# Kernel tuning notes

Hardware: AMD Instinct MI355X
Metric: run time of the kernel (lower is better)

The kernel has to match this reference:

```python
import jax, jax.numpy as jnp
import numpy as np

# Loihi neuron / simulation constants (params['neuron'], params['simulation'])
VTH_MANT = 80
V_DECAY = 128
I_DECAY = 1024
REF_DELAY = 1
WGT_EXP = 0
TAU_RHO = 1.0
SCALE_RHO = 1.0
TS = 1
THETA = float(VTH_MANT * (1 << 6))      # 5120, Loihi threshold in fixed-point units
W_SCALE = float(1 << (6 + WGT_EXP))     # 64, weight scaling into Loihi fixed point


def st_floor(x):
    """floor with straight-through gradient (Loihi integer truncation)."""
    return x + jax.lax.stop_gradient(jnp.floor(x) - x)


@jax.custom_vjp
def spike_fn(v):
    # binary spike scaled by 1/Ts, as in SLAYER-Loihi
    return (v >= THETA).astype(v.dtype) * (1.0 / TS)

def _spike_fwd(v):
    return spike_fn(v), v

def _spike_bwd(v, g):
    # SLAYER surrogate: scaleRho/(tauRho*theta) * exp(-|v - theta| / (tauRho*theta))
    pdf = (SCALE_RHO / (TAU_RHO * THETA)) * jnp.exp(-jnp.abs(v - THETA) / (TAU_RHO * THETA))
    return (g * pdf,)

spike_fn.defvjp(_spike_fwd, _spike_bwd)


def quantize_w(w, step=2.0):
    """SLAYER snn.utils.quantize(w, 2) with straight-through gradient."""
    return w + jax.lax.stop_gradient(jnp.round(w / step) * step - w)


def loihi_spikes(wsp):
    """Loihi CUBA neuron scan. wsp: [T, B, C] weighted spike input -> [T, B, C] spikes."""
    i_mul = (4096.0 - I_DECAY) / 4096.0
    v_mul = (4096.0 - V_DECAY) / 4096.0

    def step(carry, x):
        I, V, ref = carry
        I = st_floor(I * i_mul) + W_SCALE * x
        V = st_floor(V * v_mul) + I
        V = jnp.where(ref > 0, jnp.zeros_like(V), V)   # refractory hold at 0
        s = spike_fn(V)
        V = V * (1.0 - s * TS)                          # reset to 0 on spike
        ref = jnp.where(s > 0, REF_DELAY - 1, jnp.maximum(ref - 1, 0))
        return (I, V, ref), s

    B, C = wsp.shape[1], wsp.shape[2]
    init = (jnp.zeros((B, C), wsp.dtype),
            jnp.zeros((B, C), wsp.dtype),
            jnp.zeros((B, C), jnp.int32))
    _, s = jax.lax.scan(step, init, wsp)
    return s


def delay_shift(x):
    """delayShift(x, 1): shift spikes one step forward in time. x: [T, B, C]."""
    return jnp.concatenate([jnp.zeros_like(x[:1]), x[:-1]], axis=0)


def setup_inputs() -> dict:
    key = jax.random.key(0)
    k1, k2, k3 = jax.random.split(key, 3)
    B, IN, HID, OUT, T = 32, 1024, 2048, 512, 256
    spike_input = (jax.random.uniform(k1, (B, IN, T)) < 0.05).astype(jnp.float32)
    W1 = jax.random.normal(k2, (HID, IN), jnp.float32) * 8.0
    W2 = jax.random.normal(k3, (OUT, HID), jnp.float32) * 8.0
    return {"spike_input": spike_input, "W1": W1, "W2": W2}


def reference(spike_input, W1, W2):
    # spike_input: [B, IN, T] binary spikes
    x = jnp.transpose(spike_input, (2, 0, 1))          # [T, B, IN]
    w1 = quantize_w(W1)
    w2 = quantize_w(W2)
    h = jnp.einsum('tbi,hi->tbh', x, w1)               # fc1 per timestep
    s1 = delay_shift(loihi_spikes(h))                  # spikeLoihi + delayShift(1)
    o = jnp.einsum('tbh,oh->tbo', s1, w2)              # fc2 per timestep
    s2 = delay_shift(loihi_spikes(o))
    return jnp.transpose(s2, (1, 2, 0))                # [B, OUT, T]
```

## Files before the change

### kernel.cpp

```cpp
#include <hip/hip_runtime.h>

typedef unsigned char u8;
typedef signed char i8;
typedef unsigned int u32;
typedef __attribute__((ext_vector_type(4))) int i32x4;

#define AS1 __attribute__((address_space(1)))
#define AS3 __attribute__((address_space(3)))

__device__ __forceinline__ void gload_lds16(const void* g, void* l) {
    __builtin_amdgcn_global_load_lds((const AS1 void*)g, (AS3 void*)l, 16, 0, 0);
}

__global__ void prep(const float* __restrict__ X, i8* __restrict__ Xb,
                     const float4* __restrict__ W1, const float4* __restrict__ W2,
                     char4* __restrict__ W1q, char4* __restrict__ W2q) {
    const int n1v = 2048 * 1024 / 4, n2v = 512 * 2048 / 4;
    __shared__ float tile[128][33];
    int bid = blockIdx.x;
    if (bid < 3072) {
        int i = bid * 256 + threadIdx.x;
        if (i < n1v) {
            float4 w = W1[i];
            char4 q;
            q.x = (i8)(int)rintf(w.x * 0.5f);
            q.y = (i8)(int)rintf(w.y * 0.5f);
            q.z = (i8)(int)rintf(w.z * 0.5f);
            q.w = (i8)(int)rintf(w.w * 0.5f);
            W1q[i] = q;
        } else {
            int j = i - n1v;
            if (j < n2v) {
                float4 w = W2[j];
                char4 q;
                q.x = (i8)(int)rintf(w.x * 0.5f);
                q.y = (i8)(int)rintf(w.y * 0.5f);
                q.z = (i8)(int)rintf(w.z * 0.5f);
                q.w = (i8)(int)rintf(w.w * 0.5f);
                W2q[j] = q;
            }
        }
        return;
    }
    bid -= 3072;
    const int B = 32, IN = 1024, T = 256;
    const int t0 = (bid & 7) * 32, i0 = ((bid >> 3) & 7) * 128, b = bid >> 6;
    const int tx = threadIdx.x & 31, ty = threadIdx.x >> 5;
    const float* src = X + (size_t)b * IN * T;
#pragma unroll
    for (int r = 0; r < 16; ++r) {
        int i = ty + r * 8;
        tile[i][tx] = src[(size_t)(i0 + i) * T + t0 + tx];
    }
    __syncthreads();
    const int cx = threadIdx.x & 31;
    const int tl0 = threadIdx.x >> 5;
#pragma unroll
    for (int r = 0; r < 4; ++r) {
        int tl = tl0 + r * 8;
        uchar4 pk;
        pk.x = (tile[cx * 4 + 0][tl] != 0.f) ? 1 : 0;
        pk.y = (tile[cx * 4 + 1][tl] != 0.f) ? 1 : 0;
        pk.z = (tile[cx * 4 + 2][tl] != 0.f) ? 1 : 0;
        pk.w = (tile[cx * 4 + 3][tl] != 0.f) ? 1 : 0;
        *(uchar4*)&Xb[((size_t)b * T + t0 + tl) * IN + i0 + cx * 4] = pk;
    }
}

__global__ __launch_bounds__(512, 4) void gemm1_scan1(
        const i8* __restrict__ A, const i8* __restrict__ Bt,
        i8* __restrict__ S1, int K) {
    __shared__ __align__(16) i8 lds[69632];
    i8*    lA   = lds;
    i8*    lB   = lds + 32768;
    short* hT   = (short*)lds;
    u32*   bits = (u32*)(lds + 65536);

    const int nwg = gridDim.x;
    const int cpx = nwg >> 3;
    const int wg  = (blockIdx.x & 7) * cpx + (blockIdx.x >> 3);
    const int bx = wg & 15;
    const int by = wg >> 4;
    const int n0 = bx * 128;
    const int m0 = by * 256;

    const int tid  = threadIdx.x;
    const int lane = tid & 63;
    const int w    = tid >> 6;
    const int wm   = w & 3;
    const int wn   = w >> 2;
    const int l15 = lane & 15;
    const int l4  = lane >> 4;
    const int sw  = l15 & 7;

    i32x4 acc[4][4] = {};
    const int flatT = tid * 16;

    for (int k0 = 0; k0 < K; k0 += 128) {
        __syncthreads();
#pragma unroll
        for (int q = 0; q < 4; ++q) {
            int fl = q * 8192 + flatT;
            int r  = fl >> 7;
            int sc = ((fl >> 4) & 7) ^ (r & 7);
            gload_lds16(A + (size_t)(m0 + r) * K + k0 + sc * 16, &lA[fl]);
        }
#pragma unroll
        for (int q = 0; q < 2; ++q) {
            int fl = q * 8192 + flatT;
            int r  = fl >> 7;
            int sc = ((fl >> 4) & 7) ^ (r & 7);
            gload_lds16(Bt + (size_t)(n0 + r) * K + k0 + sc * 16, &lB[fl]);
        }
        __syncthreads();
#pragma unroll
        for (int kk = 0; kk < 2; ++kk) {
            i32x4 af[4], bf[4];
#pragma unroll
            for (int mf = 0; mf < 4; ++mf)
                af[mf] = *(const i32x4*)&lA[(wm * 64 + mf * 16 + l15) * 128 +
                                            ((kk * 4 + l4) ^ sw) * 16];
#pragma unroll
            for (int nf = 0; nf < 4; ++nf)
                bf[nf] = *(const i32x4*)&lB[(wn * 64 + nf * 16 + l15) * 128 +
                                            ((kk * 4 + l4) ^ sw) * 16];
#pragma unroll
            for (int mf = 0; mf < 4; ++mf)
#pragma unroll
                for (int nf = 0; nf < 4; ++nf)
                    acc[mf][nf] = __builtin_amdgcn_mfma_i32_16x16x64_i8(
                        af[mf], bf[nf], acc[mf][nf], 0, 0, 0);
        }
    }
    __syncthreads();

#pragma unroll
    for (int mf = 0; mf < 4; ++mf)
#pragma unroll
        for (int nf = 0; nf < 4; ++nf) {
            int n = wn * 64 + nf * 16 + l15;
            int c = wm * 16 + mf * 4 + l4;
            int h0 = acc[mf][nf][0] * 2, h1 = acc[mf][nf][1] * 2;
            int h2 = acc[mf][nf][2] * 2, h3 = acc[mf][nf][3] * 2;
            int2 pk;
            pk.x = (h0 & 0xffff) | (h1 << 16);
            pk.y = (h2 & 0xffff) | (h3 << 16);
            *(int2*)((char*)hT + n * 512 + ((c ^ (n & 15)) << 3)) = pk;
        }
    __syncthreads();

    {
        const int ssel = blockIdx.x & 3;
        const int w1   = 4 + ((ssel + 1) & 3);
        const int nbase = (w == ssel) ? 0 : (w == w1) ? 64 : -1;
        if (nbase >= 0) {
            const int n = nbase + lane;
            const int nx = n & 15;
            const char* hrow = (char*)hT + n * 512;
            int2 ra[4], rb[4];
#pragma unroll
            for (int q = 0; q < 4; ++q)
                ra[q] = *(const int2*)(hrow + ((q ^ nx) << 3));
            u32 bw[8] = {0, 0, 0, 0, 0, 0, 0, 0};
            float I = 0.f, V = 0.f;
#pragma unroll
            for (int p = 0; p < 16; ++p) {
                if (p < 15) {
#pragma unroll
                    for (int q = 0; q < 4; ++q) {
                        int2 v = *(const int2*)(hrow + ((((p + 1) * 4 + q) ^ nx) << 3));
                        if (p & 1) ra[q] = v; else rb[q] = v;
                    }
                }
#pragma unroll
                for (int q = 0; q < 4; ++q) {
                    int2 hh = (p & 1) ? rb[q] : ra[q];
#pragma unroll
                    for (int j = 0; j < 4; ++j) {
                        int t = p * 16 + q * 4 + j;
                        short hv = (j == 0) ? (short)hh.x
                                 : (j == 1) ? (short)(hh.x >> 16)
                                 : (j == 2) ? (short)hh.y
                                            : (short)(hh.y >> 16);
                        I = floorf(I * 0.75f) + 64.f * (float)hv;
                        V = floorf(V * 0.96875f) + I;
                        if (V >= 5120.f) { bw[t >> 5] |= (1u << (t & 31)); V = 0.f; }
                    }
                }
            }
#pragma unroll
            for (int wi = 0; wi < 8; ++wi) bits[wi * 128 + n] = bw[wi];
        }
    }
    __syncthreads();

#pragma unroll
    for (int rep = 0; rep < 16; ++rep) {
        int d   = rep * 512 + tid;
        int tt  = d >> 5;
        int ndq = d & 31;
        u32 outw = 0;
        if (tt > 0) {
            int tb = tt - 1, wi = tb >> 5, sh = tb & 31;
            outw =  ((bits[wi * 128 + ndq * 4 + 0] >> sh) & 1)
                 | (((bits[wi * 128 + ndq * 4 + 1] >> sh) & 1) << 8)
                 | (((bits[wi * 128 + ndq * 4 + 2] >> sh) & 1) << 16)
                 | (((bits[wi * 128 + ndq * 4 + 3] >> sh) & 1) << 24);
        }
        *(u32*)&S1[(size_t)(m0 + tt) * 2048 + n0 + ndq * 4] = outw;
    }
}

__global__ __launch_bounds__(512, 2) void gemm2_scan2(
        const i8* __restrict__ A, const i8* __restrict__ Bt,
        float* __restrict__ out) {
    const int K = 2048;
    __shared__ __align__(16) i8 lds[81920];
    float* hT   = (float*)lds;
    u32*   bits = (u32*)(lds + 65536);

    const int nwg = gridDim.x;
    const int cpx = nwg >> 3;
    const int wg  = (blockIdx.x & 7) * cpx + (blockIdx.x >> 3);
    const int scanw = blockIdx.x & 7;
    const int ox = wg & 7;
    const int by = wg >> 3;
    const int n0 = ox * 64;
    const int m0 = by * 256;

    const int tid  = threadIdx.x;
    const int lane = tid & 63;
    const int w    = tid >> 6;
    const int wm   = w & 3;
    const int wn   = w >> 2;
    const int l15 = lane & 15;
    const int l4  = lane >> 4;
    const int sw  = l15 & 7;

    i32x4 acc[4][2] = {};

    auto STAGE = [&](int buf, int k0) {
        i8* lA = lds + buf * 40960;
        i8* lB = lA + 32768;
#pragma unroll
        for (int q = 0; q < 4; ++q) {
            int fl = q * 8192 + tid * 16;
            int r  = fl >> 7;
            int sc = ((fl >> 4) & 7) ^ (r & 7);
            gload_lds16(A + (size_t)(m0 + r) * K + k0 + sc * 16, &lA[fl]);
        }
        {
            int fl = tid * 16;
            int r  = fl >> 7;
            int sc = ((fl >> 4) & 7) ^ (r & 7);
            gload_lds16(Bt + (size_t)(n0 + r) * K + k0 + sc * 16, &lB[fl]);
        }
    };

    auto COMPUTE = [&](int buf) {
        const i8* lA = lds + buf * 40960;
        const i8* lB = lA + 32768;
#pragma unroll
        for (int kk = 0; kk < 2; ++kk) {
            i32x4 af[4], bf[2];
#pragma unroll
            for (int mf = 0; mf < 4; ++mf)
                af[mf] = *(const i32x4*)&lA[(wm * 64 + mf * 16 + l15) * 128 +
                                            ((kk * 4 + l4) ^ sw) * 16];
#pragma unroll
            for (int nf = 0; nf < 2; ++nf)
                bf[nf] = *(const i32x4*)&lB[(wn * 32 + nf * 16 + l15) * 128 +
                                            ((kk * 4 + l4) ^ sw) * 16];
#pragma unroll
            for (int mf = 0; mf < 4; ++mf)
#pragma unroll
                for (int nf = 0; nf < 2; ++nf)
                    acc[mf][nf] = __builtin_amdgcn_mfma_i32_16x16x64_i8(
                        af[mf], bf[nf], acc[mf][nf], 0, 0, 0);
        }
    };

    STAGE(0, 0);
    __syncthreads();
    int cur = 0;
    for (int k0 = 0; k0 < K; k0 += 128) {
        if (k0 + 128 < K) STAGE(cur ^ 1, k0 + 128);
        COMPUTE(cur);
        __syncthreads();
        cur ^= 1;
    }

#pragma unroll
    for (int mf = 0; mf < 4; ++mf)
#pragma unroll
        for (int nf = 0; nf < 2; ++nf) {
            int n = wn * 32 + nf * 16 + l15;
            int c = wm * 16 + mf * 4 + l4;
            float4 pk;
            pk.x = (float)(acc[mf][nf][0] * 2);
            pk.y = (float)(acc[mf][nf][1] * 2);
            pk.z = (float)(acc[mf][nf][2] * 2);
            pk.w = (float)(acc[mf][nf][3] * 2);
            *(float4*)((char*)hT + n * 1024 + ((c ^ (n & 15)) << 4)) = pk;
        }
    __syncthreads();

    if (w == scanw) {
        const int n = lane;
        const int nx = n & 15;
        const char* hrow = (char*)hT + n * 1024;
        float4 ra[4], rb[4];
#pragma unroll
        for (int q = 0; q < 4; ++q)
            ra[q] = *(const float4*)(hrow + ((q ^ nx) << 4));
        u32 bw[8] = {0, 0, 0, 0, 0, 0, 0, 0};
        float I = 0.f, V = 0.f;
#pragma unroll
        for (int p = 0; p < 16; ++p) {
            if (p < 15) {
#pragma unroll
                for (int q = 0; q < 4; ++q) {
                    float4 v = *(const float4*)(hrow + ((((p + 1) * 4 + q) ^ nx) << 4));
                    if (p & 1) ra[q] = v; else rb[q] = v;
                }
            }
#pragma unroll
            for (int q = 0; q < 4; ++q) {
                float4 hh = (p & 1) ? rb[q] : ra[q];
#pragma unroll
                for (int j = 0; j < 4; ++j) {
                    int t = p * 16 + q * 4 + j;
                    float hv = (j == 0) ? hh.x : (j == 1) ? hh.y
                             : (j == 2) ? hh.z : hh.w;
                    I = floorf(I * 0.75f) + 64.f * hv;
                    V = floorf(V * 0.96875f) + I;
                    if (V >= 5120.f) { bw[t >> 5] |= (1u << (t & 31)); V = 0.f; }
                }
            }
        }
#pragma unroll
        for (int wi = 0; wi < 8; ++wi) bits[wi * 64 + n] = bw[wi];
    }
    __syncthreads();

#pragma unroll
    for (int rep = 0; rep < 8; ++rep) {
        int flat = rep * 512 + tid;
        int o  = flat >> 6;
        int t4 = flat & 63;
        float4 v;
#pragma unroll
        for (int j = 0; j < 4; ++j) {
            int tt = t4 * 4 + j;
            float s = 0.f;
            if (tt > 0) {
                int tb = tt - 1;
                s = (float)((bits[(tb >> 5) * 64 + o] >> (tb & 31)) & 1);
            }
            if (j == 0) v.x = s; else if (j == 1) v.y = s;
            else if (j == 2) v.z = s; else v.w = s;
        }
        *(float4*)&out[((size_t)by * 512 + n0 + o) * 256 + t4 * 4] = v;
    }
}

extern "C" void kernel_launch(void* const* d_in, const int* in_sizes, int n_in,
                              void* d_out, int out_size, void* d_ws, size_t ws_size,
                              hipStream_t stream) {
    const int B = 32, IN = 1024, HID = 2048, OUT = 512, T = 256;
    const float* spikes = (const float*)d_in[0];
    const float* W1 = (const float*)d_in[1];
    const float* W2 = (const float*)d_in[2];
    float* out = (float*)d_out;

    char* ws = (char*)d_ws;
    size_t off = 0;
    auto alloc = [&](size_t bytes) -> void* {
        void* p = ws + off;
        off += (bytes + 255) & ~(size_t)255;
        return p;
    };
    i8* Xb  = (i8*)alloc((size_t)B * T * IN);
    i8* W1q = (i8*)alloc((size_t)HID * IN);
    i8* W2q = (i8*)alloc((size_t)OUT * HID);
    i8* S1  = (i8*)alloc((size_t)B * T * HID);

    prep<<<dim3(5120), dim3(256), 0, stream>>>(
        spikes, Xb, (const float4*)W1, (const float4*)W2,
        (char4*)W1q, (char4*)W2q);
    gemm1_scan1<<<dim3(512), dim3(512), 0, stream>>>(Xb, W1q, S1, IN);
    gemm2_scan2<<<dim3(256), dim3(512), 0, stream>>>(S1, W2q, out);
}
```

Before: 62.16 us.

## Triple-buffer GEMM1 K-loop with async LDS loads and vmcnt waits

Replaces the single-buffered 128-wide K loop in gemm1_scan1 with a three-stage ring of 64-wide K tiles. Global-to-LDS loads are issued three tiles ahead and waited on with explicit vmcnt counts, so memory latency overlaps MFMA work. The loop is fully unrolled with a hardcoded K=1024, uses a new XOR swizzle and raises wave priority around the MFMA groups. LDS use grows to 77824 bytes, which may cut occupancy, and the kernel now works only for K=1024.

```diff
diff --git a/kernel.cpp b/kernel.cpp
--- a/kernel.cpp
+++ b/kernel.cpp
@@ -10,6 +10,13 @@
 
 __device__ __forceinline__ void gload_lds16(const void* g, void* l) {
     __builtin_amdgcn_global_load_lds((const AS1 void*)g, (AS3 void*)l, 16, 0, 0);
+}
+
+template <int N>
+__device__ __forceinline__ void vm_wait() {
+    if constexpr (N == 0)      asm volatile("s_waitcnt vmcnt(0)" ::: "memory");
+    else if constexpr (N == 3) asm volatile("s_waitcnt vmcnt(3)" ::: "memory");
+    else if constexpr (N == 6) asm volatile("s_waitcnt vmcnt(6)" ::: "memory");
 }
 
 __global__ void prep(const float* __restrict__ X, i8* __restrict__ Xb,
@@ -69,12 +76,11 @@
 
 __global__ __launch_bounds__(512, 4) void gemm1_scan1(
         const i8* __restrict__ A, const i8* __restrict__ Bt,
-        i8* __restrict__ S1, int K) {
-    __shared__ __align__(16) i8 lds[69632];
-    i8*    lA   = lds;
-    i8*    lB   = lds + 32768;
+        i8* __restrict__ S1) {
+    const int K = 1024;
+    __shared__ __align__(16) i8 lds[77824];
     short* hT   = (short*)lds;
-    u32*   bits = (u32*)(lds + 65536);
+    u32*   bits = (u32*)(lds + 73728);
 
     const int nwg = gridDim.x;
     const int cpx = nwg >> 3;
@@ -91,46 +97,78 @@
     const int wn   = w >> 2;
     const int l15 = lane & 15;
     const int l4  = lane >> 4;
-    const int sw  = l15 & 7;
+    const int sw  = (l15 >> 1) & 3;
 
     i32x4 acc[4][4] = {};
-    const int flatT = tid * 16;
-
-    for (int k0 = 0; k0 < K; k0 += 128) {
-        __syncthreads();
-#pragma unroll
-        for (int q = 0; q < 4; ++q) {
-            int fl = q * 8192 + flatT;
-            int r  = fl >> 7;
-            int sc = ((fl >> 4) & 7) ^ (r & 7);
+
+    auto STAGE = [&](int p, int kt) {
+        i8* lA = lds + p * 24576;
+        i8* lB = lA + 16384;
+        const int k0 = kt * 64;
+#pragma unroll
+        for (int q = 0; q < 2; ++q) {
+            int fl = q * 8192 + tid * 16;
+            int r  = fl >> 6;
+            int sc = ((fl >> 4) & 3) ^ ((r >> 1) & 3);
             gload_lds16(A + (size_t)(m0 + r) * K + k0 + sc * 16, &lA[fl]);
         }
-#pragma unroll
-        for (int q = 0; q < 2; ++q) {
-            int fl = q * 8192 + flatT;
-            int r  = fl >> 7;
-            int sc = ((fl >> 4) & 7) ^ (r & 7);
+        {
+            int fl = tid * 16;
+            int r  = fl >> 6;
+            int sc = ((fl >> 4) & 3) ^ ((r >> 1) & 3);
             gload_lds16(Bt + (size_t)(n0 + r) * K + k0 + sc * 16, &lB[fl]);
         }
-        __syncthreads();
-#pragma unroll
-        for (int kk = 0; kk < 2; ++kk) {
-            i32x4 af[4], bf[4];
-#pragma unroll
-            for (int mf = 0; mf < 4; ++mf)
-                af[mf] = *(const i32x4*)&lA[(wm * 64 + mf * 16 + l15) * 128 +
-                                            ((kk * 4 + l4) ^ sw) * 16];
-#pragma unroll
-            for (int nf = 0; nf < 4; ++nf)
-                bf[nf] = *(const i32x4*)&lB[(wn * 64 + nf * 16 + l15) * 128 +
-                                            ((kk * 4 + l4) ^ sw) * 16];
-#pragma unroll
-            for (int mf = 0; mf < 4; ++mf)
-#pragma unroll
-                for (int nf = 0; nf < 4; ++nf)
-                    acc[mf][nf] = __builtin_amdgcn_mfma_i32_16x16x64_i8(
-                        af[mf], bf[nf], acc[mf][nf], 0, 0, 0);
-        }
+    };
+
+    STAGE(0, 0);
+    STAGE(1, 1);
+    STAGE(2, 2);
+
+#pragma unroll
+    for (int t = 0; t < 16; ++t) {
+        if (t <= 13)      vm_wait<6>();
+        else if (t == 14) vm_wait<3>();
+        else              vm_wait<0>();
+        __builtin_amdgcn_s_barrier();
+        __builtin_amdgcn_sched_barrier(0);
+
+        const i8* lA = lds + (t % 3) * 24576;
+        const i8* lB = lA + 16384;
+        const int co = ((l4 ^ sw) << 4);
+
+        i32x4 bf0 = *(const i32x4*)&lB[(wn * 64 +  0 + l15) * 64 + co];
+        i32x4 bf1 = *(const i32x4*)&lB[(wn * 64 + 16 + l15) * 64 + co];
+        i32x4 bf2 = *(const i32x4*)&lB[(wn * 64 + 32 + l15) * 64 + co];
+        i32x4 bf3 = *(const i32x4*)&lB[(wn * 64 + 48 + l15) * 64 + co];
+        i32x4 af0 = *(const i32x4*)&lA[(wm * 64 +  0 + l15) * 64 + co];
+        i32x4 af1 = *(const i32x4*)&lA[(wm * 64 + 16 + l15) * 64 + co];
+        __builtin_amdgcn_s_setprio(1);
+        acc[0][0] = __builtin_amdgcn_mfma_i32_16x16x64_i8(af0, bf0, acc[0][0], 0, 0, 0);
+        acc[0][1] = __builtin_amdgcn_mfma_i32_16x16x64_i8(af0, bf1, acc[0][1], 0, 0, 0);
+        acc[0][2] = __builtin_amdgcn_mfma_i32_16x16x64_i8(af0, bf2, acc[0][2], 0, 0, 0);
+        acc[0][3] = __builtin_amdgcn_mfma_i32_16x16x64_i8(af0, bf3, acc[0][3], 0, 0, 0);
+        acc[1][0] = __builtin_amdgcn_mfma_i32_16x16x64_i8(af1, bf0, acc[1][0], 0, 0, 0);
+        acc[1][1] = __builtin_amdgcn_mfma_i32_16x16x64_i8(af1, bf1, acc[1][1], 0, 0, 0);
+        acc[1][2] = __builtin_amdgcn_mfma_i32_16x16x64_i8(af1, bf2, acc[1][2], 0, 0, 0);
+        acc[1][3] = __builtin_amdgcn_mfma_i32_16x16x64_i8(af1, bf3, acc[1][3], 0, 0, 0);
+        __builtin_amdgcn_s_setprio(0);
+
+        i32x4 af2 = *(const i32x4*)&lA[(wm * 64 + 32 + l15) * 64 + co];
+        i32x4 af3 = *(const i32x4*)&lA[(wm * 64 + 48 + l15) * 64 + co];
+        __builtin_amdgcn_s_setprio(1);
+        acc[2][0] = __builtin_amdgcn_mfma_i32_16x16x64_i8(af2, bf0, acc[2][0], 0, 0, 0);
+        acc[2][1] = __builtin_amdgcn_mfma_i32_16x16x64_i8(af2, bf1, acc[2][1], 0, 0, 0);
+        acc[2][2] = __builtin_amdgcn_mfma_i32_16x16x64_i8(af2, bf2, acc[2][2], 0, 0, 0);
+        acc[2][3] = __builtin_amdgcn_mfma_i32_16x16x64_i8(af2, bf3, acc[2][3], 0, 0, 0);
+        acc[3][0] = __builtin_amdgcn_mfma_i32_16x16x64_i8(af3, bf0, acc[3][0], 0, 0, 0);
+        acc[3][1] = __builtin_amdgcn_mfma_i32_16x16x64_i8(af3, bf1, acc[3][1], 0, 0, 0);
+        acc[3][2] = __builtin_amdgcn_mfma_i32_16x16x64_i8(af3, bf2, acc[3][2], 0, 0, 0);
+        acc[3][3] = __builtin_amdgcn_mfma_i32_16x16x64_i8(af3, bf3, acc[3][3], 0, 0, 0);
+        __builtin_amdgcn_s_setprio(0);
+
+        __builtin_amdgcn_sched_barrier(0);
+        __builtin_amdgcn_s_barrier();
+        if (t + 3 < 16) STAGE(t % 3, t + 3);
     }
     __syncthreads();
 
@@ -388,6 +426,6 @@
     prep<<<dim3(5120), dim3(256), 0, stream>>>(
         spikes, Xb, (const float4*)W1, (const float4*)W2,
         (char4*)W1q, (char4*)W2q);
-    gemm1_scan1<<<dim3(512), dim3(512), 0, stream>>>(Xb, W1q, S1, IN);
+    gemm1_scan1<<<dim3(512), dim3(512), 0, stream>>>(Xb, W1q, S1);
     gemm2_scan2<<<dim3(256), dim3(512), 0, stream>>>(S1, W2q, out);
 }
```

Measured after the change: 63.07 us. No clear change (+1.5%).
